# Performance work log

Hardware: AMD Instinct MI355X
Metric: run time of the kernel (lower is better)

The kernel has to match this reference:

```python
import jax, jax.numpy as jnp
import numpy as np

T, B, H, IN = 512, 128, 1024, 64  # IN = input_dim (x_feat=63 plus 1 feedback channel)
INIT_OUT = 1e-9


def setup_inputs() -> dict:
    key = jax.random.key(0)
    ks = jax.random.split(key, 8)
    s_ih = 1.0 / np.sqrt(H)
    return {
        "x": jax.random.normal(ks[0], (T, B, IN - 1), dtype=jnp.float32),
        # torch nn.LSTM params, gate order i,f,g,o stacked along dim 0
        "W_ih": jax.random.uniform(ks[1], (4 * H, IN), dtype=jnp.float32, minval=-s_ih, maxval=s_ih),
        "W_hh": jax.random.uniform(ks[2], (4 * H, H), dtype=jnp.float32, minval=-s_ih, maxval=s_ih),
        "b_ih": jax.random.uniform(ks[3], (4 * H,), dtype=jnp.float32, minval=-s_ih, maxval=s_ih),
        "b_hh": jax.random.uniform(ks[4], (4 * H,), dtype=jnp.float32, minval=-s_ih, maxval=s_ih),
        # nn.Linear(hidden_dim, 1)
        "W_lin": jax.random.uniform(ks[5], (1, H), dtype=jnp.float32, minval=-s_ih, maxval=s_ih),
        "b_lin": jax.random.uniform(ks[6], (1,), dtype=jnp.float32, minval=-s_ih, maxval=s_ih),
    }


def _forward(x, W_ih, W_hh, b_ih, b_hh, W_lin, b_lin):
    b = b_ih + b_hh

    def step(carry, xt):
        h, c, prev_out = carry  # h,c: (B,H); prev_out: (B,)
        inp = jnp.concatenate([xt, prev_out[:, None]], axis=1)  # (B, IN)
        gates = inp @ W_ih.T + h @ W_hh.T + b                   # (B, 4H)
        i, f, g, o = jnp.split(gates, 4, axis=1)
        c = jax.nn.sigmoid(f) * c + jax.nn.sigmoid(i) * jnp.tanh(g)
        h = jax.nn.sigmoid(o) * jnp.tanh(c)
        out = (h @ W_lin.T + b_lin)[:, 0]                        # (B,)
        return (h, c, out), out

    h0 = jnp.zeros((B, H), x.dtype)
    c0 = jnp.zeros((B, H), x.dtype)
    out0 = jnp.full((B,), INIT_OUT, x.dtype)
    _, outs = jax.lax.scan(step, (h0, c0, out0), x[1:])          # (T-1, B)
    return jnp.concatenate([out0[None, :], outs], axis=0)        # (T, B)


def reference(x, W_ih, W_hh, b_ih, b_hh, W_lin, b_lin):
    return _forward(x, W_ih, W_hh, b_ih, b_hh, W_lin, b_lin)
```

## Files before the change

kernel.cpp:

```cpp
#include <hip/hip_runtime.h>
#include <stdint.h>


typedef short short8 __attribute__((ext_vector_type(8)));
typedef float float4v __attribute__((ext_vector_type(4)));
typedef int int4v __attribute__((ext_vector_type(4)));
typedef int int2v __attribute__((ext_vector_type(2)));

#define KP 1152
#define ZROW 2320

__device__ __forceinline__ unsigned short f2bf(float f) {
  unsigned int u = __float_as_uint(f);
  u += 0x7fffu + ((u >> 16) & 1u);
  return (unsigned short)(u >> 16);
}
__device__ __forceinline__ float sigm(float x) { return 1.0f / (1.0f + __expf(-x)); }
__device__ __forceinline__ float tanh_f(float x) {
  float ax = fabsf(x);
  float e = __expf(-2.0f * ax);
  float r = (1.0f - e) / (1.0f + e);
  return x < 0.0f ? -r : r;
}

__global__ void prep_w(const float* __restrict__ W_ih, const float* __restrict__ W_hh,
                       const float* __restrict__ W_lin, const float* __restrict__ b_ih,
                       const float* __restrict__ b_hh, const float* __restrict__ b_lin,
                       unsigned short* __restrict__ Wcat, float* __restrict__ b1,
                       float* __restrict__ b2) {
  int idx = blockIdx.x * 256 + threadIdx.x;
  if (idx < 4096 * KP) {
    int j = idx / KP;
    int k = idx - j * KP;
    float v = 0.0f;
    if (k < 63) v = W_ih[j * 64 + k];
    else if (k >= 64 && k < 1088) {
      int kk = k - 64;
      v = W_hh[j * 1024 + kk] + W_ih[j * 64 + 63] * W_lin[kk];
    }
    Wcat[idx] = f2bf(v);
  }
  if (idx < 4096) {
    float wfb = W_ih[idx * 64 + 63];
    float base = b_ih[idx] + b_hh[idx];
    b1[idx] = base + 1e-9f * wfb;
    b2[idx] = base + b_lin[0] * wfb;
  }
}

__global__ void prep_x(const float* __restrict__ x, unsigned short* __restrict__ xbf) {
  int idx = blockIdx.x * 256 + threadIdx.x;
  int c = idx & 63;
  int bi = idx >> 6;
  unsigned short v = 0;
  if (c < 63) v = f2bf(x[bi * 63 + c]);
  xbf[idx] = v;
}

__global__ void initk(unsigned int* __restrict__ Hz, int* __restrict__ flags) {
  int idx = blockIdx.x * 256 + threadIdx.x;
  Hz[idx] = 0u;
  Hz[idx + 65536] = 0u;
  if (idx < 1024) flags[idx] = 0;
}

__global__ __launch_bounds__(256, 1) void lstm_rec(
    const unsigned short* __restrict__ Wcat, const unsigned short* __restrict__ xbf,
    const float* __restrict__ b1, const float* __restrict__ b2,
    const float* __restrict__ Wlin, unsigned short* __restrict__ Hbuf,
    float* __restrict__ outp, int* __restrict__ flags) {
  const int tid = threadIdx.x;
  const int bid = blockIdx.x;
  const int g = bid & 7;
  const int mb = bid >> 3;
  const int wv = tid >> 6;
  const int ln = tid & 63;
  const int lr = ln & 15;
  const int lq = ln >> 4;
  const int rp = wv * 2 + (ln >> 5);
  const int c = ln & 31;

  __shared__ __align__(16) char zs[16 * ZROW];
  __shared__ __align__(16) float pbuf[4][8][16][20];

#pragma unroll
  for (int s = 0; s < 10; ++s) {
    int i = s * 256 + tid;
    if (i < 16 * ZROW / 16) {
      int4v z = {0, 0, 0, 0};
      *reinterpret_cast<int4v*>(zs + i * 16) = z;
    }
  }
  __syncthreads();

  short8 bf[8][9];
#pragma unroll
  for (int n = 0; n < 8; ++n) {
    const unsigned short* wrow =
        Wcat + (size_t)((n >> 1) * 1024 + mb * 32 + (n & 1) * 16 + lr) * KP;
#pragma unroll
    for (int j = 0; j < 9; ++j)
      bf[n][j] = *reinterpret_cast<const short8*>(wrow + (wv * 9 + j) * 32 + lq * 8);
  }

  const int gcb = mb * 32 + c;
  float bias2[4];
#pragma unroll
  for (int q = 0; q < 4; ++q) bias2[q] = b2[q * 1024 + gcb];
  const float wl = Wlin[gcb];
  float cs0 = 0.f, cs1 = 0.f;

  for (int t = 1; t < 512; ++t) {
    const int tm1 = t - 1;
    if (t > 1) {
      const int* fp = flags + g * 128 + ln * 2;
      int guard = 0;
      for (;;) {
        int2v ff;
        asm volatile("global_load_dwordx2 %0, %1, off sc0 sc1\n\ts_waitcnt vmcnt(0)"
                     : "=v"(ff) : "v"(fp) : "memory");
        if (__all((ff.x >= tm1) && (ff.y >= tm1))) break;
        if (++guard > (1 << 18)) break;
      }
    }

    const unsigned short* hsrc =
        Hbuf + ((t - 1) & 1) * 131072 + (size_t)(g * 16) * 1024;
    const unsigned short* xsrc = xbf + (size_t)t * 8192 + (size_t)(g * 16) * 64;
    int4v tmp[8];
#pragma unroll
    for (int s = 0; s < 8; ++s) {
      int hc = s * 256 + tid;
      const unsigned short* p = hsrc + (hc >> 7) * 1024 + (hc & 127) * 8;
      asm volatile("global_load_dwordx4 %0, %1, off sc0 sc1" : "=v"(tmp[s]) : "v"(p));
    }
    int4v xv;
    if (tid < 128)
      asm volatile("global_load_dwordx4 %0, %1, off"
                   : "=v"(xv) : "v"(xsrc + (tid >> 3) * 64 + (tid & 7) * 8));
    asm volatile("s_waitcnt vmcnt(0)" ::: "memory");
    __builtin_amdgcn_sched_barrier(0);
#pragma unroll
    for (int s = 0; s < 8; ++s) {
      int hc = s * 256 + tid;
      *reinterpret_cast<int4v*>(zs + (hc >> 7) * ZROW + 128 + (hc & 127) * 16) = tmp[s];
    }
    if (tid < 128)
      *reinterpret_cast<int4v*>(zs + (tid >> 3) * ZROW + (tid & 7) * 16) = xv;
    __syncthreads();

    float4v acc[8];
#pragma unroll
    for (int n = 0; n < 8; ++n) acc[n] = (float4v){0.f, 0.f, 0.f, 0.f};
#pragma unroll
    for (int j = 0; j < 9; ++j) {
      const short8 a = *reinterpret_cast<const short8*>(
          zs + lr * ZROW + (wv * 9 + j) * 64 + lq * 16);
#pragma unroll
      for (int n = 0; n < 8; ++n)
        acc[n] = __builtin_amdgcn_mfma_f32_16x16x32_bf16(a, bf[n][j], acc[n], 0, 0, 0);
    }
#pragma unroll
    for (int n = 0; n < 8; ++n)
      *reinterpret_cast<float4v*>(&pbuf[wv][n][lr][lq * 4]) = acc[n];
    __syncthreads();

    float ga0[4], ga1[4];
    const int nlo = c >> 4;
    const int cc = c & 15;
#pragma unroll
    for (int q = 0; q < 4; ++q) {
      float s0 = 0.f, s1 = 0.f;
#pragma unroll
      for (int w2 = 0; w2 < 4; ++w2) {
        const float* pp = &pbuf[w2][q * 2 + nlo][cc][2 * rp];
        s0 += pp[0];
        s1 += pp[1];
      }
      ga0[q] = s0;
      ga1[q] = s1;
    }
    float lb0 = bias2[0], lb1 = bias2[1], lb2 = bias2[2], lb3 = bias2[3];
    if (t == 1) {
      lb0 = b1[gcb];
      lb1 = b1[1024 + gcb];
      lb2 = b1[2048 + gcb];
      lb3 = b1[3072 + gcb];
    }
    float i0 = sigm(ga0[0] + lb0), f0 = sigm(ga0[1] + lb1);
    float G0 = tanh_f(ga0[2] + lb2), o0 = sigm(ga0[3] + lb3);
    float i1 = sigm(ga1[0] + lb0), f1 = sigm(ga1[1] + lb1);
    float G1 = tanh_f(ga1[2] + lb2), o1 = sigm(ga1[3] + lb3);
    cs0 = f0 * cs0 + i0 * G0;
    cs1 = f1 * cs1 + i1 * G1;
    float h0v = o0 * tanh_f(cs0);
    float h1v = o1 * tanh_f(cs1);

    unsigned short* Hd = Hbuf + (t & 1) * 131072;
    const int r0 = g * 16 + rp * 2;
    unsigned short* p0 = Hd + (size_t)r0 * 1024 + gcb;
    unsigned short* p1 = p0 + 1024;
    int hb0 = (int)f2bf(h0v), hb1 = (int)f2bf(h1v);
    asm volatile("global_store_short %0, %1, off sc0 sc1" :: "v"(p0), "v"(hb0) : "memory");
    asm volatile("global_store_short %0, %1, off sc0 sc1" :: "v"(p1), "v"(hb1) : "memory");
    asm volatile("s_waitcnt vmcnt(0)" ::: "memory");
    if (ln == 0) {
      int* fp2 = flags + g * 128 + mb * 4 + wv;
      asm volatile("global_store_dword %0, %1, off sc0 sc1" :: "v"(fp2), "v"(t) : "memory");
    }

    float pa = h0v * wl, pb = h1v * wl;
    pa += __shfl_xor(pa, 1); pb += __shfl_xor(pb, 1);
    pa += __shfl_xor(pa, 2); pb += __shfl_xor(pb, 2);
    pa += __shfl_xor(pa, 4); pb += __shfl_xor(pb, 4);
    pa += __shfl_xor(pa, 8); pb += __shfl_xor(pb, 8);
    pa += __shfl_xor(pa, 16); pb += __shfl_xor(pb, 16);
    if (c == 0) {
      outp[(size_t)(t * 128 + r0) * 32 + mb] = pa;
      outp[(size_t)(t * 128 + r0 + 1) * 32 + mb] = pb;
    }
  }
}

__global__ void finalize(const float* __restrict__ outp, const float* __restrict__ b_lin,
                         float* __restrict__ out) {
  int tid = threadIdx.x;
  int ln = tid & 63;
  int wv = tid >> 6;
  int half = ln >> 5;
  int lane = ln & 31;
  int row = blockIdx.x * 8 + wv * 2 + half;
  float v = outp[(size_t)row * 32 + lane];
  v += __shfl_xor(v, 1);
  v += __shfl_xor(v, 2);
  v += __shfl_xor(v, 4);
  v += __shfl_xor(v, 8);
  v += __shfl_xor(v, 16);
  if (lane == 0) out[row] = (row < 128) ? 1e-9f : (v + b_lin[0]);
}

extern "C" void kernel_launch(void* const* d_in, const int* in_sizes, int n_in,
                              void* d_out, int out_size, void* d_ws, size_t ws_size,
                              hipStream_t stream) {
  const float* x = (const float*)d_in[0];
  const float* W_ih = (const float*)d_in[1];
  const float* W_hh = (const float*)d_in[2];
  const float* b_ih = (const float*)d_in[3];
  const float* b_hh = (const float*)d_in[4];
  const float* W_lin = (const float*)d_in[5];
  const float* b_lin = (const float*)d_in[6];
  float* out = (float*)d_out;

  char* ws = (char*)d_ws;
  const size_t WS_WCAT = 0;
  const size_t WS_XBF  = 9437184;
  const size_t WS_B1   = 17825792;
  const size_t WS_B2   = 17842176;
  const size_t WS_H    = 17858560;
  const size_t WS_OUTP = 18382848;
  const size_t WS_FLAG = 26771456;
  if (ws_size < WS_FLAG + 4096) return;

  unsigned short* Wcat = (unsigned short*)(ws + WS_WCAT);
  unsigned short* xbf = (unsigned short*)(ws + WS_XBF);
  float* b1 = (float*)(ws + WS_B1);
  float* b2 = (float*)(ws + WS_B2);
  unsigned short* Hbuf = (unsigned short*)(ws + WS_H);
  float* outp = (float*)(ws + WS_OUTP);
  int* flags = (int*)(ws + WS_FLAG);

  prep_w<<<18432, 256, 0, stream>>>(W_ih, W_hh, W_lin, b_ih, b_hh, b_lin, Wcat, b1, b2);
  prep_x<<<16384, 256, 0, stream>>>(x, xbf);
  initk<<<256, 256, 0, stream>>>((unsigned int*)Hbuf, flags);
  lstm_rec<<<256, 256, 0, stream>>>(Wcat, xbf, b1, b2, W_lin, Hbuf, outp, flags);
  finalize<<<8192, 256, 0, stream>>>(outp, b_lin, out);
}
```

Before: 1.987 ms.

## Load MFMA A-fragments directly from global, drop LDS staging and one barrier

```diff
diff --git a/kernel.cpp b/kernel.cpp
--- a/kernel.cpp
+++ b/kernel.cpp
@@ -5,10 +5,8 @@
 typedef short short8 __attribute__((ext_vector_type(8)));
 typedef float float4v __attribute__((ext_vector_type(4)));
 typedef int int4v __attribute__((ext_vector_type(4)));
-typedef int int2v __attribute__((ext_vector_type(2)));
 
 #define KP 1152
-#define ZROW 2320
 
 __device__ __forceinline__ unsigned short f2bf(float f) {
   unsigned int u = __float_as_uint(f);
@@ -80,18 +78,7 @@
   const int rp = wv * 2 + (ln >> 5);
   const int c = ln & 31;
 
-  __shared__ __align__(16) char zs[16 * ZROW];
-  __shared__ __align__(16) float pbuf[4][8][16][20];
-
-#pragma unroll
-  for (int s = 0; s < 10; ++s) {
-    int i = s * 256 + tid;
-    if (i < 16 * ZROW / 16) {
-      int4v z = {0, 0, 0, 0};
-      *reinterpret_cast<int4v*>(zs + i * 16) = z;
-    }
-  }
-  __syncthreads();
+  __shared__ __align__(16) float pbuf[2][4][8][16][20];
 
   short8 bf[8][9];
 #pragma unroll
@@ -102,6 +89,24 @@
     for (int j = 0; j < 9; ++j)
       bf[n][j] = *reinterpret_cast<const short8*>(wrow + (wv * 9 + j) * 32 + lq * 8);
   }
+#pragma unroll
+  for (int n = 0; n < 8; ++n)
+#pragma unroll
+    for (int j = 0; j < 9; ++j)
+      asm volatile("" : "+v"(bf[n][j]));
+
+  const int kb = wv * 9;
+  const int jlo = (kb < 2) ? 2 : 0;
+  const int jhi = (kb + 9 > 34) ? 7 : 9;
+  const int pmin = (kb < 2) ? 0 : kb - 2;
+  const int pmax = (kb + 6 < 31) ? kb + 6 : 31;
+  const int cnt = 4 * (pmax - pmin + 1);
+  const int* fp = flags + g * 128 + 4 * pmin + ((ln < cnt) ? ln : cnt - 1);
+
+  int hoff[9];
+#pragma unroll
+  for (int j = 0; j < 9; ++j)
+    hoff[j] = ((g * 16 + lr) * 1024 + (kb + j - 2) * 32 + lq * 8) * 2;
 
   const int gcb = mb * 32 + c;
   float bias2[4];
@@ -112,57 +117,52 @@
 
   for (int t = 1; t < 512; ++t) {
     const int tm1 = t - 1;
+    short8 xa0, xa1;
+    if (kb == 0) {
+      const unsigned short* xrow =
+          xbf + (size_t)t * 8192 + (g * 16 + lr) * 64 + lq * 8;
+      xa0 = *reinterpret_cast<const short8*>(xrow);
+      xa1 = *reinterpret_cast<const short8*>(xrow + 32);
+    }
+
     if (t > 1) {
-      const int* fp = flags + g * 128 + ln * 2;
       int guard = 0;
       for (;;) {
-        int2v ff;
-        asm volatile("global_load_dwordx2 %0, %1, off sc0 sc1\n\ts_waitcnt vmcnt(0)"
-                     : "=v"(ff) : "v"(fp) : "memory");
-        if (__all((ff.x >= tm1) && (ff.y >= tm1))) break;
+        int v;
+        asm volatile("global_load_dword %0, %1, off sc0 sc1\n\ts_waitcnt vmcnt(0)"
+                     : "=v"(v) : "v"(fp) : "memory");
+        if (__all(v >= tm1)) break;
         if (++guard > (1 << 18)) break;
       }
     }
 
-    const unsigned short* hsrc =
-        Hbuf + ((t - 1) & 1) * 131072 + (size_t)(g * 16) * 1024;
-    const unsigned short* xsrc = xbf + (size_t)t * 8192 + (size_t)(g * 16) * 64;
-    int4v tmp[8];
-#pragma unroll
-    for (int s = 0; s < 8; ++s) {
-      int hc = s * 256 + tid;
-      const unsigned short* p = hsrc + (hc >> 7) * 1024 + (hc & 127) * 8;
-      asm volatile("global_load_dwordx4 %0, %1, off sc0 sc1" : "=v"(tmp[s]) : "v"(p));
-    }
-    int4v xv;
-    if (tid < 128)
-      asm volatile("global_load_dwordx4 %0, %1, off"
-                   : "=v"(xv) : "v"(xsrc + (tid >> 3) * 64 + (tid & 7) * 8));
+    const unsigned short* hb = Hbuf + ((t - 1) & 1) * 131072;
+    short8 af[9];
+    if (kb == 0) { af[0] = xa0; af[1] = xa1; }
+    if (jhi == 7) {
+      short8 z8 = {0, 0, 0, 0, 0, 0, 0, 0};
+      af[7] = z8; af[8] = z8;
+    }
+#pragma unroll
+    for (int j = 0; j < 9; ++j)
+      if (j >= jlo && j < jhi)
+        asm volatile("global_load_dwordx4 %0, %1, %2 sc0 sc1"
+                     : "=v"(af[j]) : "v"(hoff[j]), "s"(hb));
     asm volatile("s_waitcnt vmcnt(0)" ::: "memory");
     __builtin_amdgcn_sched_barrier(0);
-#pragma unroll
-    for (int s = 0; s < 8; ++s) {
-      int hc = s * 256 + tid;
-      *reinterpret_cast<int4v*>(zs + (hc >> 7) * ZROW + 128 + (hc & 127) * 16) = tmp[s];
-    }
-    if (tid < 128)
-      *reinterpret_cast<int4v*>(zs + (tid >> 3) * ZROW + (tid & 7) * 16) = xv;
-    __syncthreads();
 
     float4v acc[8];
 #pragma unroll
     for (int n = 0; n < 8; ++n) acc[n] = (float4v){0.f, 0.f, 0.f, 0.f};
 #pragma unroll
-    for (int j = 0; j < 9; ++j) {
-      const short8 a = *reinterpret_cast<const short8*>(
-          zs + lr * ZROW + (wv * 9 + j) * 64 + lq * 16);
+    for (int j = 0; j < 9; ++j)
 #pragma unroll
       for (int n = 0; n < 8; ++n)
-        acc[n] = __builtin_amdgcn_mfma_f32_16x16x32_bf16(a, bf[n][j], acc[n], 0, 0, 0);
-    }
+        acc[n] = __builtin_amdgcn_mfma_f32_16x16x32_bf16(af[j], bf[n][j], acc[n], 0, 0, 0);
+
 #pragma unroll
     for (int n = 0; n < 8; ++n)
-      *reinterpret_cast<float4v*>(&pbuf[wv][n][lr][lq * 4]) = acc[n];
+      *reinterpret_cast<float4v*>(&pbuf[t & 1][wv][n][lr][lq * 4]) = acc[n];
     __syncthreads();
 
     float ga0[4], ga1[4];
@@ -173,7 +173,7 @@
       float s0 = 0.f, s1 = 0.f;
 #pragma unroll
       for (int w2 = 0; w2 < 4; ++w2) {
-        const float* pp = &pbuf[w2][q * 2 + nlo][cc][2 * rp];
+        const float* pp = &pbuf[t & 1][w2][q * 2 + nlo][cc][2 * rp];
         s0 += pp[0];
         s1 += pp[1];
       }
```

Measured after the change: 2.086 ms. +5.0%, slower.
